# Performance work log

Measured on AMD Instinct MI355X. Metric: run time of the kernel, lower is better.

Reference implementation:

```python
import jax, jax.numpy as jnp
import numpy as np

N_HEADS = 16
INPUT_DIM = 1024
EMBED_DIM = 1024
KEY_DIM = EMBED_DIM // N_HEADS  # 64, val_dim == key_dim
BATCH = 4
SEQ = 2048


def _uniform(key, shape, bound):
    return jax.random.uniform(key, shape, jnp.float32, -bound, bound)


def setup_inputs() -> dict:
    key = jax.random.key(0)
    kq, k1, k2, k3, k4 = jax.random.split(key, 5)
    stdv_k = 1.0 / np.sqrt(KEY_DIM)
    stdv_e = 1.0 / np.sqrt(EMBED_DIM)
    return {
        "q": jax.random.normal(kq, (BATCH, SEQ, INPUT_DIM), jnp.float32),
        "W_query": _uniform(k1, (N_HEADS, INPUT_DIM, KEY_DIM), stdv_k),
        "W_key": _uniform(k2, (N_HEADS, INPUT_DIM, KEY_DIM), stdv_k),
        "W_val": _uniform(k3, (N_HEADS, INPUT_DIM, KEY_DIM), stdv_k),
        "W_out": _uniform(k4, (N_HEADS, KEY_DIM, EMBED_DIM), stdv_e),
    }


def reference(q, W_query, W_key, W_val, W_out):
    # Self-attention: h = q. Project per head: [H, B, S, dk]
    norm = 1.0 / np.sqrt(KEY_DIM)
    Q = jnp.einsum("bsd,hdk->hbsk", q, W_query)
    K = jnp.einsum("bsd,hdk->hbsk", q, W_key)
    V = jnp.einsum("bsd,hdv->hbsv", q, W_val)
    # compatibility: [H, B, S_q, S_k]
    scores = norm * jnp.einsum("hbqk,hbnk->hbqn", Q, K)
    attn = jax.nn.softmax(scores, axis=-1)
    heads = jnp.einsum("hbqn,hbnv->hbqv", attn, V)
    # combine heads with per-head output projection: [B, S, E]
    out = jnp.einsum("hbqv,hve->bqe", heads, W_out)
    return out
```

## Files before the change

kernel.cpp:

```cpp
#include <hip/hip_runtime.h>
#include <hip/hip_bf16.h>
#include <stdint.h>
#include <math.h>

#define BATCH 4
#define SEQ   2048
#define NHEAD 16
#define DIM   1024
#define DKV   64
#define MTOT  (BATCH*SEQ)

typedef __attribute__((ext_vector_type(8))) short  bf16x8;
typedef __attribute__((ext_vector_type(4))) float  f32x4;
typedef unsigned short u16;
typedef unsigned int   u32;
typedef __attribute__((ext_vector_type(2))) u32 u32x2;
typedef __attribute__((ext_vector_type(4))) u32 u32x4;

#define QSCALE 0.18033688011112042f
#define THR    8.0f

__device__ __forceinline__ u16 f2bf(float f) {
  __hip_bfloat16 h = __float2bfloat16(f);
  u16 r;
  __builtin_memcpy(&r, &h, 2);
  return r;
}
__device__ __forceinline__ u32 pkbf(float lo, float hi) {
  __hip_bfloat162 h = __float22bfloat162_rn(float2{lo, hi});
  u32 r;
  __builtin_memcpy(&r, &h, 4);
  return r;
}

__device__ __forceinline__ void gload_lds16(const void* g, void* l) {
  __builtin_amdgcn_global_load_lds((u32 __attribute__((address_space(1)))*)(g),
                                   (u32 __attribute__((address_space(3)))*)(l),
                                   16, 0, 0);
}


__global__ void k_cvt_q(const float* __restrict__ src, u16* __restrict__ dst) {
  const int i = (blockIdx.x * 256 + threadIdx.x) * 4;
  float4 v = *(const float4*)(src + i);
  u32x2 o;
  o[0] = pkbf(v.x, v.y); o[1] = pkbf(v.z, v.w);
  *(u32x2*)(dst + i) = o;
}

__global__ void k_cvt_wproj(const float* __restrict__ w, u16* __restrict__ wt) {
  const int idx = blockIdx.x * 256 + threadIdx.x;
  const int n = idx >> 10, d = idx & 1023;
  wt[idx] = f2bf(w[((n >> 6) << 16) + (d << 6) + (n & 63)]);
}

__global__ void k_cvt_wout(const float* __restrict__ w, u16* __restrict__ wt) {
  const int idx = blockIdx.x * 256 + threadIdx.x;
  const int e = idx >> 10, hv = idx & 1023;
  wt[idx] = f2bf(w[(hv << 10) + e]);
}


template<int MODE>
__device__ __forceinline__ void gemm2(u16* __restrict__ sm,
                                      const u16* __restrict__ A, const u16* __restrict__ Bt,
                                      void* __restrict__ Cp, int m0, int n0) {
  const int tid = threadIdx.x, wid = tid >> 6, lane = tid & 63;
  const int g = lane >> 4, li = lane & 15;
  const int wm = wid >> 1, wn = wid & 1;

  const int c0 = wid * 128 + lane, c1 = c0 + 64;
  const int s0 = (c0 * 8) ^ (((c0 >> 3) & 7) << 3);
  const int s1 = (c1 * 8) ^ (((c1 >> 3) & 7) << 3);
  const int cB = tid;
  const int sB = (cB * 8) ^ (((cB >> 3) & 7) << 3);
  const u16* As0 = A  + (size_t)(m0 + (s0 >> 5)) * DIM + (s0 & 31);
  const u16* As1 = A  + (size_t)(m0 + (s1 >> 5)) * DIM + (s1 & 31);
  const u16* Bs  = Bt + (size_t)(n0 + (sB >> 5)) * DIM + (sB & 31);
  u16* dA0 = sm + wid * 1024;
  u16* dA1 = sm + wid * 1024 + 512;
  u16* dB  = sm + 32768 + wid * 512;

#define SA2(t, ks, tb) do { \
    gload_lds16(As0 + (t) * 64 + (ks) * 32, dA0 + (tb) * 16384 + (ks) * 8192); \
    gload_lds16(As1 + (t) * 64 + (ks) * 32, dA1 + (tb) * 16384 + (ks) * 8192); } while (0)
#define SB2(t, ks, tb) \
    gload_lds16(Bs + (t) * 64 + (ks) * 32, dB + (tb) * 8192 + (ks) * 4096)

  const int vx = ((li >> 1) & 7) << 3;
  const int a_rd = (((wm * 64 + li) * 32) + g * 8) ^ vx;
  const int b_rd = (((wn * 64 + li) * 32) + g * 8) ^ vx;

  f32x4 acc[4][4] = {};

  SA2(0, 0, 0); SB2(0, 0, 0);
  SA2(0, 1, 0); SB2(0, 1, 0);
  SA2(1, 0, 1); SB2(1, 0, 1);
  asm volatile("s_waitcnt vmcnt(6)" ::: "memory");
  __builtin_amdgcn_s_barrier();

#pragma unroll 2
  for (int kt = 0; kt < 16; ++kt) {
    const int cur = kt & 1, t1 = (kt + 1) & 15, t2 = (kt + 2) & 15;
    const u16* pa = sm + cur * 16384 + a_rd;
    const u16* pb = sm + 32768 + cur * 8192 + b_rd;
    bf16x8 af[2], bfq[4];

#pragma unroll
    for (int j = 0; j < 4; ++j) bfq[j] = *(const bf16x8*)(pb + j * 512);
    af[0] = *(const bf16x8*)(pa);
    af[1] = *(const bf16x8*)(pa + 512);
    SA2(t1, 1, cur ^ 1);
    __builtin_amdgcn_s_barrier();
    __builtin_amdgcn_s_setprio(1);
#pragma unroll
    for (int i = 0; i < 2; ++i)
#pragma unroll
      for (int j = 0; j < 4; ++j)
        acc[i][j] = __builtin_amdgcn_mfma_f32_16x16x32_bf16(af[i], bfq[j], acc[i][j], 0, 0, 0);
    __builtin_amdgcn_s_setprio(0);
    __builtin_amdgcn_s_barrier();

    af[0] = *(const bf16x8*)(pa + 2 * 512);
    af[1] = *(const bf16x8*)(pa + 3 * 512);
    SB2(t1, 1, cur ^ 1);
    __builtin_amdgcn_s_barrier();
    __builtin_amdgcn_s_setprio(1);
#pragma unroll
    for (int i = 0; i < 2; ++i)
#pragma unroll
      for (int j = 0; j < 4; ++j)
        acc[i + 2][j] = __builtin_amdgcn_mfma_f32_16x16x32_bf16(af[i], bfq[j], acc[i + 2][j], 0, 0, 0);
    __builtin_amdgcn_s_setprio(0);
    asm volatile("s_waitcnt vmcnt(3)" ::: "memory");
    __builtin_amdgcn_s_barrier();

#pragma unroll
    for (int j = 0; j < 4; ++j) bfq[j] = *(const bf16x8*)(pb + 4096 + j * 512);
    af[0] = *(const bf16x8*)(pa + 8192);
    af[1] = *(const bf16x8*)(pa + 8192 + 512);
    SA2(t2, 0, cur);
    __builtin_amdgcn_s_barrier();
    __builtin_amdgcn_s_setprio(1);
#pragma unroll
    for (int i = 0; i < 2; ++i)
#pragma unroll
      for (int j = 0; j < 4; ++j)
        acc[i][j] = __builtin_amdgcn_mfma_f32_16x16x32_bf16(af[i], bfq[j], acc[i][j], 0, 0, 0);
    __builtin_amdgcn_s_setprio(0);
    __builtin_amdgcn_s_barrier();

    af[0] = *(const bf16x8*)(pa + 8192 + 2 * 512);
    af[1] = *(const bf16x8*)(pa + 8192 + 3 * 512);
    SB2(t2, 0, cur);
    __builtin_amdgcn_s_barrier();
    __builtin_amdgcn_s_setprio(1);
#pragma unroll
    for (int i = 0; i < 2; ++i)
#pragma unroll
      for (int j = 0; j < 4; ++j)
        acc[i + 2][j] = __builtin_amdgcn_mfma_f32_16x16x32_bf16(af[i], bfq[j], acc[i + 2][j], 0, 0, 0);
    __builtin_amdgcn_s_setprio(0);
    asm volatile("s_waitcnt vmcnt(3)" ::: "memory");
    __builtin_amdgcn_s_barrier();
  }
#undef SA2
#undef SB2

#pragma unroll
  for (int i = 0; i < 4; ++i)
#pragma unroll
    for (int j = 0; j < 4; ++j) {
      const int col = n0 + wn * 64 + j * 16 + li;
      if (MODE == 3) {
        const size_t rowb = (size_t)(m0 + wm * 64 + i * 16 + g * 4) + 4 * g - 12 * (i & 1);
        u32x2 w;
        w[0] = pkbf(acc[i][j][0], acc[i][j][1]);
        w[1] = pkbf(acc[i][j][2], acc[i][j][3]);
        *(u32x2*)((u16*)Cp + (size_t)col * MTOT + rowb) = w;
      } else if (MODE == 1) {
#pragma unroll
        for (int r = 0; r < 4; ++r) {
          const size_t row = (size_t)(m0 + wm * 64 + i * 16 + g * 4 + r);
          ((float*)Cp)[row * DIM + col] = acc[i][j][r];
        }
      } else {
#pragma unroll
        for (int r = 0; r < 4; ++r) {
          const size_t row = (size_t)(m0 + wm * 64 + i * 16 + g * 4 + r);
          float v = acc[i][j][r];
          if (MODE == 2) v *= QSCALE;
          ((u16*)Cp)[row * DIM + col] = f2bf(v);
        }
      }
    }
}

__global__ __launch_bounds__(512, 2)
void k_gemm_qkv2(const u16* __restrict__ A, const u16* __restrict__ wq,
                 const u16* __restrict__ wk, const u16* __restrict__ wv,
                 u16* __restrict__ Qo, u16* __restrict__ Ko, u16* __restrict__ Vto) {
  __shared__ u16 sm[49152];
  const int m0 = blockIdx.x * 256;
  const int yt = blockIdx.y;
  const int wsel = yt >> 3;
  const int n0 = (yt & 7) * 128;
  if (wsel == 0)      gemm2<2>(sm, A, wq, Qo,  m0, n0);
  else if (wsel == 1) gemm2<0>(sm, A, wk, Ko,  m0, n0);
  else                gemm2<3>(sm, A, wv, Vto, m0, n0);
}

__global__ __launch_bounds__(512, 2)
void k_gemm_out2(const u16* __restrict__ A, const u16* __restrict__ Bt, float* __restrict__ C) {
  __shared__ u16 sm[49152];
  gemm2<1>(sm, A, Bt, C, blockIdx.x * 256, blockIdx.y * 128);
}


#define KB 64
#define NT (SEQ/KB)

__global__ __launch_bounds__(512, 8)
void k_attn(const u16* __restrict__ Q, const u16* __restrict__ K,
            const u16* __restrict__ Vt, u16* __restrict__ O) {
  const int id = blockIdx.x;
  const int bh = id & 63, qt = id >> 6;
  const int b = bh >> 4, h = bh & 15;
  const int q0 = qt * 128;
  const int tid = threadIdx.x, wid = tid >> 6, lane = tid & 63;
  const int g = lane >> 4, li = lane & 15;

  __shared__ u16 kl[2][KB * 64];
  __shared__ u16 vl[2][KB * 64];

  const size_t rb = (size_t)b * SEQ;
  const int hc = h * DKV;

  bf16x8 qf0, qf1;
  {
    const u16* qp = Q + (rb + q0 + wid * 16 + li) * DIM + hc;
    qf0 = *(const bf16x8*)(qp + g * 8);
    qf1 = *(const bf16x8*)(qp + 32 + g * 8);
  }

  bf16x8 ones;
#pragma unroll
  for (int j = 0; j < 8; ++j) ones[j] = (short)0x3F80;

  float mrun = -1e30f, lrun = 0.f;
  f32x4 o[4] = {};

  const int r8   = lane >> 3;
  const int swz  = ((lane & 7) ^ r8) * 8;
  const int srow = wid * 8 + r8;

  gload_lds16(K  + (rb + srow) * DIM + hc + swz,          &kl[0][wid * 512]);
  gload_lds16(Vt + (size_t)(hc + srow) * MTOT + rb + swz, &vl[0][wid * 512]);

  for (int it = 0; it < NT; ++it) {
    const int cur = it & 1;
    __syncthreads();

    if (it + 1 < NT) {
      const int n1 = (it + 1) * KB;
      gload_lds16(K  + (rb + n1 + srow) * DIM + hc + swz,          &kl[cur ^ 1][wid * 512]);
      gload_lds16(Vt + (size_t)(hc + srow) * MTOT + rb + n1 + swz, &vl[cur ^ 1][wid * 512]);
    }

    const u16* kb = kl[cur];
    const u16* vb = vl[cur];
    const int sw = (li & 7) << 3;

    f32x4 s[4];
    __builtin_amdgcn_s_setprio(1);
#pragma unroll
    for (int t = 0; t < 4; ++t) {
      const int row = t * 16 + li;
      bf16x8 kf0 = *(const bf16x8*)(kb + row * 64 + ((g * 8) ^ sw));
      bf16x8 kf1 = *(const bf16x8*)(kb + row * 64 + ((32 + g * 8) ^ sw));
      f32x4 z = {};
      z = __builtin_amdgcn_mfma_f32_16x16x32_bf16(kf0, qf0, z, 0, 0, 0);
      z = __builtin_amdgcn_mfma_f32_16x16x32_bf16(kf1, qf1, z, 0, 0, 0);
      s[t] = z;
    }
    __builtin_amdgcn_s_setprio(0);

    f32x4 mv = __builtin_elementwise_max(__builtin_elementwise_max(s[0], s[1]),
                                         __builtin_elementwise_max(s[2], s[3]));
    const float lmax = fmaxf(fmaxf(mv[0], mv[1]), fmaxf(mv[2], mv[3]));
    if (__any(lmax - mrun > THR)) {
      float pmax = fmaxf(lmax, __shfl_xor(lmax, 16));
      pmax = fmaxf(pmax, __shfl_xor(pmax, 32));
      const float mn = fmaxf(mrun, pmax);
      const float corr = __builtin_amdgcn_exp2f(mrun - mn);
      mrun = mn;
      lrun *= corr;
#pragma unroll
      for (int t = 0; t < 4; ++t) o[t] *= corr;
    }
    const float mb = mrun;
#pragma unroll
    for (int t = 0; t < 4; ++t)
#pragma unroll
      for (int r = 0; r < 4; ++r)
        s[t][r] = __builtin_amdgcn_exp2f(s[t][r] - mb);

    bf16x8 pa[2];
#pragma unroll
    for (int hh = 0; hh < 2; ++hh) {
      u32x4 pw;
      pw[0] = pkbf(s[2 * hh][0],     s[2 * hh][1]);
      pw[1] = pkbf(s[2 * hh][2],     s[2 * hh][3]);
      pw[2] = pkbf(s[2 * hh + 1][0], s[2 * hh + 1][1]);
      pw[3] = pkbf(s[2 * hh + 1][2], s[2 * hh + 1][3]);
      pa[hh] = __builtin_bit_cast(bf16x8, pw);
    }

    f32x4 zs = {};
    zs = __builtin_amdgcn_mfma_f32_16x16x32_bf16(ones, pa[0], zs, 0, 0, 0);
    zs = __builtin_amdgcn_mfma_f32_16x16x32_bf16(ones, pa[1], zs, 0, 0, 0);

    __builtin_amdgcn_s_setprio(1);
#pragma unroll
    for (int t = 0; t < 4; ++t) {
      const int row = t * 16 + li;
#pragma unroll
      for (int hh = 0; hh < 2; ++hh) {
        bf16x8 vf = *(const bf16x8*)(vb + row * 64 + ((hh * 32 + g * 8) ^ sw));
        o[t] = __builtin_amdgcn_mfma_f32_16x16x32_bf16(vf, pa[hh], o[t], 0, 0, 0);
      }
    }
    __builtin_amdgcn_s_setprio(0);

    lrun += zs[0];
  }

  {
    const float inv = 1.0f / lrun;
    const size_t qrow = rb + q0 + wid * 16 + li;
#pragma unroll
    for (int t = 0; t < 4; ++t) {
      u32x2 w;
      w[0] = pkbf(o[t][0] * inv, o[t][1] * inv);
      w[1] = pkbf(o[t][2] * inv, o[t][3] * inv);
      *(u32x2*)(O + qrow * DIM + hc + t * 16 + 4 * g) = w;
    }
  }
}


extern "C" void kernel_launch(void* const* d_in, const int* in_sizes, int n_in,
                              void* d_out, int out_size, void* d_ws, size_t ws_size,
                              hipStream_t stream) {
  (void)in_sizes; (void)n_in; (void)out_size; (void)ws_size;
  const float* q  = (const float*)d_in[0];
  const float* Wq = (const float*)d_in[1];
  const float* Wk = (const float*)d_in[2];
  const float* Wv = (const float*)d_in[3];
  const float* Wo = (const float*)d_in[4];
  float* out = (float*)d_out;

  char* p = (char*)d_ws;
  u16* qb  = (u16*)p; p += (size_t)MTOT * DIM * 2;
  u16* wqt = (u16*)p; p += (size_t)DIM * DIM * 2;
  u16* wkt = (u16*)p; p += (size_t)DIM * DIM * 2;
  u16* wvt = (u16*)p; p += (size_t)DIM * DIM * 2;
  u16* wot = (u16*)p; p += (size_t)DIM * DIM * 2;
  u16* Qb  = (u16*)p; p += (size_t)MTOT * DIM * 2;
  u16* Kb  = (u16*)p; p += (size_t)MTOT * DIM * 2;
  u16* Vtb = (u16*)p; p += (size_t)MTOT * DIM * 2;
  u16* Hb  = Qb;

  k_cvt_q<<<(MTOT * DIM / 4) / 256, 256, 0, stream>>>(q, qb);
  k_cvt_wproj<<<(DIM * DIM) / 256, 256, 0, stream>>>(Wq, wqt);
  k_cvt_wproj<<<(DIM * DIM) / 256, 256, 0, stream>>>(Wk, wkt);
  k_cvt_wproj<<<(DIM * DIM) / 256, 256, 0, stream>>>(Wv, wvt);
  k_cvt_wout<<<(DIM * DIM) / 256, 256, 0, stream>>>(Wo, wot);

  k_gemm_qkv2<<<dim3(MTOT / 256, 24), 512, 0, stream>>>(qb, wqt, wkt, wvt, Qb, Kb, Vtb);
  k_attn<<<(SEQ / 128) * BATCH * NHEAD, 512, 0, stream>>>(Qb, Kb, Vtb, Hb);
  k_gemm_out2<<<dim3(MTOT / 256, DIM / 128), 512, 0, stream>>>(Hb, wot, out);
}
```

Before: 209.0 us.

## Process two query tiles per warp in attention to reuse K/V fragments

Each warp now handles 32 query rows (two 16-row sub-tiles) instead of 16, so each attention block covers 256 queries and the grid is halved. Every K and V fragment read from LDS feeds two MFMAs, which cuts LDS traffic and global K/V reloads per query. In exchange register pressure roughly doubles for the accumulators and scores, the occupancy hint drops from 8 to 4 blocks, and there are fewer blocks (512) to spread across the CUs.

```diff
diff --git a/kernel.cpp b/kernel.cpp
--- a/kernel.cpp
+++ b/kernel.cpp
@@ -220,13 +220,13 @@
 #define KB 64
 #define NT (SEQ/KB)
 
-__global__ __launch_bounds__(512, 8)
+__global__ __launch_bounds__(512, 4)
 void k_attn(const u16* __restrict__ Q, const u16* __restrict__ K,
             const u16* __restrict__ Vt, u16* __restrict__ O) {
   const int id = blockIdx.x;
   const int bh = id & 63, qt = id >> 6;
   const int b = bh >> 4, h = bh & 15;
-  const int q0 = qt * 128;
+  const int q0 = qt * 256;
   const int tid = threadIdx.x, wid = tid >> 6, lane = tid & 63;
   const int g = lane >> 4, li = lane & 15;
 
@@ -236,19 +236,21 @@
   const size_t rb = (size_t)b * SEQ;
   const int hc = h * DKV;
 
-  bf16x8 qf0, qf1;
-  {
-    const u16* qp = Q + (rb + q0 + wid * 16 + li) * DIM + hc;
-    qf0 = *(const bf16x8*)(qp + g * 8);
-    qf1 = *(const bf16x8*)(qp + 32 + g * 8);
+  bf16x8 qf[2][2];
+#pragma unroll
+  for (int u = 0; u < 2; ++u) {
+    const u16* qp = Q + (rb + q0 + wid * 32 + u * 16 + li) * DIM + hc;
+    qf[u][0] = *(const bf16x8*)(qp + g * 8);
+    qf[u][1] = *(const bf16x8*)(qp + 32 + g * 8);
   }
 
   bf16x8 ones;
 #pragma unroll
   for (int j = 0; j < 8; ++j) ones[j] = (short)0x3F80;
 
-  float mrun = -1e30f, lrun = 0.f;
-  f32x4 o[4] = {};
+  float mrun[2] = {-1e30f, -1e30f};
+  float lrun[2] = {0.f, 0.f};
+  f32x4 o[2][4] = {};
 
   const int r8   = lane >> 3;
   const int swz  = ((lane & 7) ^ r8) * 8;
@@ -271,54 +273,61 @@
     const u16* vb = vl[cur];
     const int sw = (li & 7) << 3;
 
-    f32x4 s[4];
+    f32x4 s[2][4];
     __builtin_amdgcn_s_setprio(1);
 #pragma unroll
     for (int t = 0; t < 4; ++t) {
       const int row = t * 16 + li;
       bf16x8 kf0 = *(const bf16x8*)(kb + row * 64 + ((g * 8) ^ sw));
       bf16x8 kf1 = *(const bf16x8*)(kb + row * 64 + ((32 + g * 8) ^ sw));
-      f32x4 z = {};
-      z = __builtin_amdgcn_mfma_f32_16x16x32_bf16(kf0, qf0, z, 0, 0, 0);
-      z = __builtin_amdgcn_mfma_f32_16x16x32_bf16(kf1, qf1, z, 0, 0, 0);
-      s[t] = z;
-    }
-    __builtin_amdgcn_s_setprio(0);
-
-    f32x4 mv = __builtin_elementwise_max(__builtin_elementwise_max(s[0], s[1]),
-                                         __builtin_elementwise_max(s[2], s[3]));
-    const float lmax = fmaxf(fmaxf(mv[0], mv[1]), fmaxf(mv[2], mv[3]));
-    if (__any(lmax - mrun > THR)) {
-      float pmax = fmaxf(lmax, __shfl_xor(lmax, 16));
-      pmax = fmaxf(pmax, __shfl_xor(pmax, 32));
-      const float mn = fmaxf(mrun, pmax);
-      const float corr = __builtin_amdgcn_exp2f(mrun - mn);
-      mrun = mn;
-      lrun *= corr;
-#pragma unroll
-      for (int t = 0; t < 4; ++t) o[t] *= corr;
-    }
-    const float mb = mrun;
-#pragma unroll
-    for (int t = 0; t < 4; ++t)
-#pragma unroll
-      for (int r = 0; r < 4; ++r)
-        s[t][r] = __builtin_amdgcn_exp2f(s[t][r] - mb);
-
-    bf16x8 pa[2];
-#pragma unroll
-    for (int hh = 0; hh < 2; ++hh) {
-      u32x4 pw;
-      pw[0] = pkbf(s[2 * hh][0],     s[2 * hh][1]);
-      pw[1] = pkbf(s[2 * hh][2],     s[2 * hh][3]);
-      pw[2] = pkbf(s[2 * hh + 1][0], s[2 * hh + 1][1]);
-      pw[3] = pkbf(s[2 * hh + 1][2], s[2 * hh + 1][3]);
-      pa[hh] = __builtin_bit_cast(bf16x8, pw);
-    }
-
-    f32x4 zs = {};
-    zs = __builtin_amdgcn_mfma_f32_16x16x32_bf16(ones, pa[0], zs, 0, 0, 0);
-    zs = __builtin_amdgcn_mfma_f32_16x16x32_bf16(ones, pa[1], zs, 0, 0, 0);
+#pragma unroll
+      for (int u = 0; u < 2; ++u) {
+        f32x4 z = {};
+        z = __builtin_amdgcn_mfma_f32_16x16x32_bf16(kf0, qf[u][0], z, 0, 0, 0);
+        z = __builtin_amdgcn_mfma_f32_16x16x32_bf16(kf1, qf[u][1], z, 0, 0, 0);
+        s[u][t] = z;
+      }
+    }
+    __builtin_amdgcn_s_setprio(0);
+
+    bf16x8 pa[2][2];
+#pragma unroll
+    for (int u = 0; u < 2; ++u) {
+      f32x4 mv = __builtin_elementwise_max(__builtin_elementwise_max(s[u][0], s[u][1]),
+                                           __builtin_elementwise_max(s[u][2], s[u][3]));
+      const float lmax = fmaxf(fmaxf(mv[0], mv[1]), fmaxf(mv[2], mv[3]));
+      if (__any(lmax - mrun[u] > THR)) {
+        float pmax = fmaxf(lmax, __shfl_xor(lmax, 16));
+        pmax = fmaxf(pmax, __shfl_xor(pmax, 32));
+        const float mn = fmaxf(mrun[u], pmax);
+        const float corr = __builtin_amdgcn_exp2f(mrun[u] - mn);
+        mrun[u] = mn;
+        lrun[u] *= corr;
+#pragma unroll
+        for (int t = 0; t < 4; ++t) o[u][t] *= corr;
+      }
+      const float mb = mrun[u];
+#pragma unroll
+      for (int t = 0; t < 4; ++t)
+#pragma unroll
+        for (int r = 0; r < 4; ++r)
+          s[u][t][r] = __builtin_amdgcn_exp2f(s[u][t][r] - mb);
+
+#pragma unroll
+      for (int hh = 0; hh < 2; ++hh) {
+        u32x4 pw;
+        pw[0] = pkbf(s[u][2 * hh][0],     s[u][2 * hh][1]);
+        pw[1] = pkbf(s[u][2 * hh][2],     s[u][2 * hh][3]);
+        pw[2] = pkbf(s[u][2 * hh + 1][0], s[u][2 * hh + 1][1]);
+        pw[3] = pkbf(s[u][2 * hh + 1][2], s[u][2 * hh + 1][3]);
+        pa[u][hh] = __builtin_bit_cast(bf16x8, pw);
+      }
+
+      f32x4 zs = {};
+      zs = __builtin_amdgcn_mfma_f32_16x16x32_bf16(ones, pa[u][0], zs, 0, 0, 0);
+      zs = __builtin_amdgcn_mfma_f32_16x16x32_bf16(ones, pa[u][1], zs, 0, 0, 0);
+      lrun[u] += zs[0];
+    }
 
     __builtin_amdgcn_s_setprio(1);
 #pragma unroll
@@ -327,22 +336,23 @@
 #pragma unroll
       for (int hh = 0; hh < 2; ++hh) {
         bf16x8 vf = *(const bf16x8*)(vb + row * 64 + ((hh * 32 + g * 8) ^ sw));
-        o[t] = __builtin_amdgcn_mfma_f32_16x16x32_bf16(vf, pa[hh], o[t], 0, 0, 0);
-      }
-    }
-    __builtin_amdgcn_s_setprio(0);
-
-    lrun += zs[0];
+#pragma unroll
+        for (int u = 0; u < 2; ++u)
+          o[u][t] = __builtin_amdgcn_mfma_f32_16x16x32_bf16(vf, pa[u][hh], o[u][t], 0, 0, 0);
+      }
+    }
+    __builtin_amdgcn_s_setprio(0);
   }
 
-  {
-    const float inv = 1.0f / lrun;
-    const size_t qrow = rb + q0 + wid * 16 + li;
+#pragma unroll
+  for (int u = 0; u < 2; ++u) {
+    const float inv = 1.0f / lrun[u];
+    const size_t qrow = rb + q0 + wid * 32 + u * 16 + li;
 #pragma unroll
     for (int t = 0; t < 4; ++t) {
       u32x2 w;
-      w[0] = pkbf(o[t][0] * inv, o[t][1] * inv);
-      w[1] = pkbf(o[t][2] * inv, o[t][3] * inv);
+      w[0] = pkbf(o[u][t][0] * inv, o[u][t][1] * inv);
+      w[1] = pkbf(o[u][t][2] * inv, o[u][t][3] * inv);
       *(u32x2*)(O + qrow * DIM + hc + t * 16 + 4 * g) = w;
     }
   }
@@ -378,6 +388,6 @@
   k_cvt_wout<<<(DIM * DIM) / 256, 256, 0, stream>>>(Wo, wot);
 
   k_gemm_qkv2<<<dim3(MTOT / 256, 24), 512, 0, stream>>>(qb, wqt, wkt, wvt, Qb, Kb, Vtb);
-  k_attn<<<(SEQ / 128) * BATCH * NHEAD, 512, 0, stream>>>(Qb, Kb, Vtb, Hb);
+  k_attn<<<(SEQ / 256) * BATCH * NHEAD, 512, 0, stream>>>(Qb, Kb, Vtb, Hb);
   k_gemm_out2<<<dim3(MTOT / 256, DIM / 128), 512, 0, stream>>>(Hb, wot, out);
 }
```

Result: no change. 207.6 us (-0.7%).
